# Kernel optimization log

Measured on AMD Instinct MI355X. Metric: run time of the kernel, lower is better.

The kernel has to match this reference:

```python
import jax, jax.numpy as jnp
import numpy as np

N_NODES = 50000
N_EDGES = 800000
A_DIM = 128
B_DIM = 128


def setup_inputs() -> dict:
    key = jax.random.key(0)
    k1, k2, k3, k4, k5, k6 = jax.random.split(key, 6)
    edge_rows = jax.random.randint(k1, (N_EDGES,), 0, N_NODES, dtype=jnp.int32)
    edge_cols = jax.random.randint(k2, (N_EDGES,), 0, N_NODES, dtype=jnp.int32)
    edge_vals = jax.random.uniform(k3, (N_EDGES,), dtype=jnp.float32)
    H = jax.random.normal(k4, (N_NODES, A_DIM), dtype=jnp.float32)
    std = 1.0 / np.sqrt(B_DIM)
    W = jax.random.uniform(k5, (A_DIM, B_DIM), minval=-std, maxval=std, dtype=jnp.float32)
    bias = jax.random.uniform(k6, (B_DIM,), minval=-std, maxval=std, dtype=jnp.float32)
    return {"edge_rows": edge_rows, "edge_cols": edge_cols, "edge_vals": edge_vals,
            "H": H, "W": W, "bias": bias}


def reference(edge_rows, edge_cols, edge_vals, H, W, bias):
    # HW = H @ W  (dense GEMM)
    HW = jnp.matmul(H, W)  # [n, b]
    # AHW = A @ HW where A is sparse COO: A[r, c] = v
    msgs = edge_vals[:, None] * HW[edge_cols]  # [nnz, b]
    AHW = jax.ops.segment_sum(msgs, edge_rows, num_segments=H.shape[0])  # [n, b]
    return AHW + bias
```

## Files before the change

kernel.cpp:

```cpp
#include <hip/hip_runtime.h>
#include <hip/hip_fp16.h>

#define ADIM 128
#define BDIM 128
#define CAP  64
#define CPAD 16
#define NT   8
#define NKS  4

typedef _Float16 half8 __attribute__((ext_vector_type(8)));
typedef float    f32x4 __attribute__((ext_vector_type(4)));
typedef unsigned int uint;
typedef unsigned short ushort;

__global__ __launch_bounds__(256) void prep_kernel(const float* __restrict__ W,
                                                   _Float16* __restrict__ Bh,
                                                   _Float16* __restrict__ Bl,
                                                   int* __restrict__ counts,
                                                   int n_cnt) {
    const int gid = blockIdx.x * 256 + threadIdx.x;
    if (blockIdx.x < 8) {
        const int l  = gid & 63;
        const int ks = (gid >> 6) & 3;
        const int t  = gid >> 8;
        const int kbase = ks * 32 + (l >> 4) * 8;
        const int col   = t * 16 + (l & 15);
        half8 hi, lo;
#pragma unroll
        for (int j = 0; j < 8; ++j) {
            const float w = W[(size_t)(kbase + j) * BDIM + col];
            const _Float16 h = (_Float16)w;
            hi[j] = h;
            lo[j] = (_Float16)(w - (float)h);
        }
        const size_t off = ((size_t)(t * NKS + ks) * 64 + l) * 8;
        *(half8*)(Bh + off) = hi;
        *(half8*)(Bl + off) = lo;
    } else {
        const int idx = gid - 2048;
        if (idx < n_cnt) counts[idx] = 0;
    }
}

__global__ __launch_bounds__(256) void fused_gemm_bucket(
        const float* __restrict__ H,
        const _Float16* __restrict__ Bh, const _Float16* __restrict__ Bl,
        _Float16* __restrict__ HWh, int n_nodes, int gemm_blocks,
        const int* __restrict__ rows, const int* __restrict__ cols,
        const float* __restrict__ vals, int* __restrict__ counts,
        uint* __restrict__ ebuf, int n_edges) {
    const int tid = threadIdx.x;

    if ((int)blockIdx.x >= gemm_blocks) {
        const int e = ((int)blockIdx.x - gemm_blocks) * 256 + tid;
        if (e < n_edges) {
            const int   r = __builtin_nontemporal_load(rows + e);
            const int   c = __builtin_nontemporal_load(cols + e);
            const float v = __builtin_nontemporal_load(vals + e);
            const int pos = atomicAdd(&counts[(size_t)r * CPAD], 1);
            if (pos < CAP)
                ebuf[(size_t)r * CAP + pos] =
                    ((uint)c << 16) | (uint)__half_as_ushort(__float2half(v));
        }
        return;
    }

    const int l     = tid & 63;
    const int w     = tid >> 6;
    const int row_m = l & 15;
    const int kq    = l >> 4;
    const int n_strips = n_nodes >> 4;

    const int s = (int)blockIdx.x * 4 + w;
    if (s >= n_strips) return;
    const int r0 = s << 4;

    f32x4 acc[NT];
#pragma unroll
    for (int t = 0; t < NT; ++t) acc[t] = (f32x4){0.f, 0.f, 0.f, 0.f};

#pragma unroll
    for (int ks = 0; ks < NKS; ++ks) {
        half8 ah, al;
        {
            const int rr = r0 + row_m;
            const float4 x =
                *(const float4*)(H + (size_t)rr * ADIM + ks * 32 + kq * 8);
            const float4 y =
                *(const float4*)(H + (size_t)rr * ADIM + ks * 32 + kq * 8 + 4);
            const float xv[8] = {x.x, x.y, x.z, x.w, y.x, y.y, y.z, y.w};
#pragma unroll
            for (int j = 0; j < 8; ++j) {
                const _Float16 h = (_Float16)xv[j];
                ah[j] = h;
                al[j] = (_Float16)(xv[j] - (float)h);
            }
        }
#pragma unroll
        for (int t = 0; t < NT; ++t) {
            const size_t off = ((size_t)(t * NKS + ks) * 64 + l) * 8;
            const half8 bh = *(const half8*)(Bh + off);
            const half8 bl = *(const half8*)(Bl + off);
            acc[t] = __builtin_amdgcn_mfma_f32_16x16x32_f16(ah, bh, acc[t], 0, 0, 0);
            acc[t] = __builtin_amdgcn_mfma_f32_16x16x32_f16(ah, bl, acc[t], 0, 0, 0);
            acc[t] = __builtin_amdgcn_mfma_f32_16x16x32_f16(al, bh, acc[t], 0, 0, 0);
        }
    }

    const int rb = r0 + kq * 4;
#pragma unroll
    for (int t = 0; t < NT; ++t)
#pragma unroll
        for (int r = 0; r < 4; ++r)
            HWh[(size_t)(rb + r) * BDIM + t * 16 + row_m] = (_Float16)acc[t][r];
}

__global__ __launch_bounds__(256) void gather_kernel(const int* __restrict__ counts,
                                                     const uint* __restrict__ ebuf,
                                                     const _Float16* __restrict__ HWh,
                                                     const float* __restrict__ bias,
                                                     float* __restrict__ out,
                                                     int n_nodes) {
    const int lane = threadIdx.x & 63;
    const int q    = lane >> 4;
    const int t    = lane & 15;
    const int node = (int)((blockIdx.x * (long)blockDim.x + threadIdx.x) >> 6);
    if (node >= n_nodes) return;

    int deg = __builtin_amdgcn_readfirstlane(counts[(size_t)node * CPAD]);
    if (deg > CAP) deg = CAP;

    const uint* ebn = ebuf + (size_t)node * CAP;

    float acc[8];
#pragma unroll
    for (int j = 0; j < 8; ++j) acc[j] = 0.f;

    for (int i0 = 0; i0 < deg; i0 += 16) {
        uint e[4];
#pragma unroll
        for (int u = 0; u < 4; ++u) {
            const int idx = i0 + q + 4 * u;
            e[u] = (idx < deg) ? ebn[idx] : 0u;
        }
        int4 h[4];
#pragma unroll
        for (int u = 0; u < 4; ++u)
            h[u] = *(const int4*)(HWh + (size_t)(e[u] >> 16) * BDIM + t * 8);
#pragma unroll
        for (int u = 0; u < 4; ++u) {
            __half_raw hr; hr.x = (ushort)(e[u] & 0xFFFFu);
            const float v = __half2float(*(__half*)&hr);
            const __half2* hp = (const __half2*)&h[u];
#pragma unroll
            for (int j = 0; j < 4; ++j) {
                const float2 f = __half22float2(hp[j]);
                acc[2 * j + 0] += f.x * v;
                acc[2 * j + 1] += f.y * v;
            }
        }
    }

#pragma unroll
    for (int j = 0; j < 8; ++j) {
        acc[j] += __shfl_xor(acc[j], 16, 64);
        acc[j] += __shfl_xor(acc[j], 32, 64);
    }

    if (q < 2) {
        const float4 b = ((const float4*)bias)[t * 2 + q];
        const float4 o = make_float4(acc[4 * q + 0] + b.x, acc[4 * q + 1] + b.y,
                                     acc[4 * q + 2] + b.z, acc[4 * q + 3] + b.w);
        *(float4*)(out + (size_t)node * BDIM + t * 8 + q * 4) = o;
    }
}

extern "C" void kernel_launch(void* const* d_in, const int* in_sizes, int n_in,
                              void* d_out, int out_size, void* d_ws, size_t ws_size,
                              hipStream_t stream) {
    const int*   edge_rows = (const int*)d_in[0];
    const int*   edge_cols = (const int*)d_in[1];
    const float* edge_vals = (const float*)d_in[2];
    const float* H         = (const float*)d_in[3];
    const float* W         = (const float*)d_in[4];
    const float* bias      = (const float*)d_in[5];

    const int n_edges = in_sizes[0];
    const int n_nodes = in_sizes[3] / ADIM;
    const int n_cnt   = n_nodes * CPAD;

    const size_t hw_bytes   = ((size_t)n_nodes * BDIM * sizeof(_Float16) + 15) & ~(size_t)15;
    const size_t cnt_bytes  = ((size_t)n_cnt * sizeof(int) + 15) & ~(size_t)15;
    const size_t ebuf_bytes = ((size_t)n_nodes * CAP * sizeof(uint) + 15) & ~(size_t)15;
    const size_t frag_bytes = (size_t)NT * NKS * 64 * 8 * sizeof(_Float16);

    char* ws = (char*)d_ws;
    _Float16* HWh  = (_Float16*)ws;  ws += hw_bytes;
    int*      cnt  = (int*)ws;       ws += cnt_bytes;
    uint*     ebuf = (uint*)ws;      ws += ebuf_bytes;
    _Float16* Bh   = (_Float16*)ws;  ws += frag_bytes;
    _Float16* Bl   = (_Float16*)ws;

    const int zero_blocks = (n_cnt + 255) / 256;
    prep_kernel<<<8 + zero_blocks, 256, 0, stream>>>(W, Bh, Bl, cnt, n_cnt);

    const int n_strips      = n_nodes >> 4;
    const int gemm_blocks   = (n_strips + 3) / 4;
    const int bucket_blocks = (n_edges + 255) / 256;
    fused_gemm_bucket<<<gemm_blocks + bucket_blocks, 256, 0, stream>>>(
        H, Bh, Bl, HWh, n_nodes, gemm_blocks,
        edge_rows, edge_cols, edge_vals, cnt, ebuf, n_edges);

    gather_kernel<<<(n_nodes + 3) / 4, 256, 0, stream>>>(cnt, ebuf, HWh, bias,
                                                         (float*)d_out, n_nodes);
}
```

Measured before the change: 163.5 us.

## Partition edge bucketing by XCD node range and drop counter padding

The bucketing phase now assigns each group of 8 consecutive blocks the same 2048-edge chunk. Each block in the group keeps only edges whose destination row falls in one eighth of the node range, chosen by blockIdx mod 8. The assumption is that blocks are dispatched round-robin to the 8 XCDs, so atomics and ebuf writes for a given row stay within one XCD's L2. Per-row counters are no longer padded to 16 ints, which shrinks the zeroing pass and the counter footprint. The cost is that every edge is loaded 8 times, plus extra filter branches. Unpadded counters may also bring back false sharing on the atomics.

Result: no change. 162.2 us (-0.8%).

```diff
diff --git a/kernel.cpp b/kernel.cpp
--- a/kernel.cpp
+++ b/kernel.cpp
@@ -4,9 +4,9 @@
 #define ADIM 128
 #define BDIM 128
 #define CAP  64
-#define CPAD 16
 #define NT   8
 #define NKS  4
+#define NXCD 8
 
 typedef _Float16 half8 __attribute__((ext_vector_type(8)));
 typedef float    f32x4 __attribute__((ext_vector_type(4)));
@@ -17,7 +17,7 @@
                                                    _Float16* __restrict__ Bh,
                                                    _Float16* __restrict__ Bl,
                                                    int* __restrict__ counts,
-                                                   int n_cnt) {
+                                                   int n_nodes) {
     const int gid = blockIdx.x * 256 + threadIdx.x;
     if (blockIdx.x < 8) {
         const int l  = gid & 63;
@@ -38,7 +38,7 @@
         *(half8*)(Bl + off) = lo;
     } else {
         const int idx = gid - 2048;
-        if (idx < n_cnt) counts[idx] = 0;
+        if (idx < n_nodes) counts[idx] = 0;
     }
 }
 
@@ -52,15 +52,45 @@
     const int tid = threadIdx.x;
 
     if ((int)blockIdx.x >= gemm_blocks) {
-        const int e = ((int)blockIdx.x - gemm_blocks) * 256 + tid;
-        if (e < n_edges) {
-            const int   r = __builtin_nontemporal_load(rows + e);
-            const int   c = __builtin_nontemporal_load(cols + e);
-            const float v = __builtin_nontemporal_load(vals + e);
-            const int pos = atomicAdd(&counts[(size_t)r * CPAD], 1);
-            if (pos < CAP)
-                ebuf[(size_t)r * CAP + pos] =
-                    ((uint)c << 16) | (uint)__half_as_ushort(__float2half(v));
+        const int pb    = (int)blockIdx.x - gemm_blocks;
+        const int cls   = (int)blockIdx.x & 7;
+        const int chunk = pb >> 3;
+        const int part  = (n_nodes + NXCD - 1) / NXCD;
+        const int lo    = cls * part;
+        const int span  = ((lo + part) < n_nodes ? part : (n_nodes - lo));
+        const int e0    = chunk * 2048 + tid * 8;
+
+        if (e0 + 8 <= n_edges) {
+            const int4   ra = *(const int4*)(rows + e0);
+            const int4   rb = *(const int4*)(rows + e0 + 4);
+            const int4   ca = *(const int4*)(cols + e0);
+            const int4   cb = *(const int4*)(cols + e0 + 4);
+            const float4 va = *(const float4*)(vals + e0);
+            const float4 vb = *(const float4*)(vals + e0 + 4);
+            const int   r8[8] = {ra.x, ra.y, ra.z, ra.w, rb.x, rb.y, rb.z, rb.w};
+            const int   c8[8] = {ca.x, ca.y, ca.z, ca.w, cb.x, cb.y, cb.z, cb.w};
+            const float v8[8] = {va.x, va.y, va.z, va.w, vb.x, vb.y, vb.z, vb.w};
+#pragma unroll
+            for (int u = 0; u < 8; ++u) {
+                if ((uint)(r8[u] - lo) < (uint)span) {
+                    const int pos = atomicAdd(&counts[r8[u]], 1);
+                    if (pos < CAP)
+                        ebuf[(size_t)r8[u] * CAP + pos] =
+                            ((uint)c8[u] << 16) |
+                            (uint)__half_as_ushort(__float2half(v8[u]));
+                }
+            }
+        } else {
+            for (int e = e0; e < n_edges; ++e) {
+                const int r = rows[e];
+                if ((uint)(r - lo) < (uint)span) {
+                    const int pos = atomicAdd(&counts[r], 1);
+                    if (pos < CAP)
+                        ebuf[(size_t)r * CAP + pos] =
+                            ((uint)cols[e] << 16) |
+                            (uint)__half_as_ushort(__float2half(vals[e]));
+                }
+            }
         }
         return;
     }
@@ -127,7 +157,7 @@
     const int node = (int)((blockIdx.x * (long)blockDim.x + threadIdx.x) >> 6);
     if (node >= n_nodes) return;
 
-    int deg = __builtin_amdgcn_readfirstlane(counts[(size_t)node * CPAD]);
+    int deg = __builtin_amdgcn_readfirstlane(counts[node]);
     if (deg > CAP) deg = CAP;
 
     const uint* ebn = ebuf + (size_t)node * CAP;
@@ -187,10 +217,9 @@
 
     const int n_edges = in_sizes[0];
     const int n_nodes = in_sizes[3] / ADIM;
-    const int n_cnt   = n_nodes * CPAD;
 
     const size_t hw_bytes   = ((size_t)n_nodes * BDIM * sizeof(_Float16) + 15) & ~(size_t)15;
-    const size_t cnt_bytes  = ((size_t)n_cnt * sizeof(int) + 15) & ~(size_t)15;
+    const size_t cnt_bytes  = ((size_t)n_nodes * sizeof(int) + 15) & ~(size_t)15;
     const size_t ebuf_bytes = ((size_t)n_nodes * CAP * sizeof(uint) + 15) & ~(size_t)15;
     const size_t frag_bytes = (size_t)NT * NKS * 64 * 8 * sizeof(_Float16);
 
@@ -201,12 +230,13 @@
     _Float16* Bh   = (_Float16*)ws;  ws += frag_bytes;
     _Float16* Bl   = (_Float16*)ws;
 
-    const int zero_blocks = (n_cnt + 255) / 256;
-    prep_kernel<<<8 + zero_blocks, 256, 0, stream>>>(W, Bh, Bl, cnt, n_cnt);
+    const int zero_blocks = (n_nodes + 255) / 256;
+    prep_kernel<<<8 + zero_blocks, 256, 0, stream>>>(W, Bh, Bl, cnt, n_nodes);
 
     const int n_strips      = n_nodes >> 4;
     const int gemm_blocks   = (n_strips + 3) / 4;
-    const int bucket_blocks = (n_edges + 255) / 256;
+    const int n_chunks      = (n_edges + 2047) / 2048;
+    const int bucket_blocks = n_chunks * NXCD;
     fused_gemm_bucket<<<gemm_blocks + bucket_blocks, 256, 0, stream>>>(
         H, Bh, Bl, HWh, n_nodes, gemm_blocks,
         edge_rows, edge_cols, edge_vals, cnt, ebuf, n_edges);
```
